# Performance work log

Hardware: AMD Instinct MI355X
Metric: run time of the kernel (lower is better)

The kernel has to match this reference:

```python
import jax, jax.numpy as jnp
import numpy as np

P = 16         # patch size
D = 192        # embed dim (vit_tiny)
NH = 3         # heads
DEPTH = 12
HID = 768      # mlp hidden = 4*D
NCLS = 1000
PCT = 0.25
EPS = 1e-6


def _ln(x, s, b):
    m = x.mean(-1, keepdims=True)
    v = ((x - m) ** 2).mean(-1, keepdims=True)
    return (x - m) * jax.lax.rsqrt(v + EPS) * s + b


def setup_inputs() -> dict:
    key = jax.random.key(0)
    ks = jax.random.split(key, 24)
    B, IMG = 64, 384
    std = 0.02
    d = {
        "magno_image": jax.random.normal(ks[0], (B, 3, IMG, IMG), jnp.float32),
        "line_drawing": jax.random.uniform(ks[1], (B, 1, IMG, IMG), jnp.float32),
        "conv_w": jax.random.normal(ks[2], (D, 3, P, P), jnp.float32) * std,
        "conv_b": jnp.zeros((D,), jnp.float32),
        "pos_embed": jax.random.normal(ks[3], (1, (IMG // P) ** 2 + 1, D), jnp.float32) * std,
        "cls_token": jax.random.normal(ks[4], (1, 1, D), jnp.float32) * std,
        "ln1_s": jnp.ones((DEPTH, D), jnp.float32),
        "ln1_b": jnp.zeros((DEPTH, D), jnp.float32),
        "qkv_w": jax.random.normal(ks[5], (DEPTH, D, 3 * D), jnp.float32) * std,
        "qkv_b": jnp.zeros((DEPTH, 3 * D), jnp.float32),
        "proj_w": jax.random.normal(ks[6], (DEPTH, D, D), jnp.float32) * std,
        "proj_b": jnp.zeros((DEPTH, D), jnp.float32),
        "ln2_s": jnp.ones((DEPTH, D), jnp.float32),
        "ln2_b": jnp.zeros((DEPTH, D), jnp.float32),
        "fc1_w": jax.random.normal(ks[7], (DEPTH, D, HID), jnp.float32) * std,
        "fc1_b": jnp.zeros((DEPTH, HID), jnp.float32),
        "fc2_w": jax.random.normal(ks[8], (DEPTH, HID, D), jnp.float32) * std,
        "fc2_b": jnp.zeros((DEPTH, D), jnp.float32),
        "normf_s": jnp.ones((D,), jnp.float32),
        "normf_b": jnp.zeros((D,), jnp.float32),
        "head_w": jax.random.normal(ks[9], (D, NCLS), jnp.float32) * std,
        "head_b": jnp.zeros((NCLS,), jnp.float32),
    }
    return d


def _forward(magno_image, line_drawing, conv_w, conv_b, pos_embed, cls_token,
             ln1_s, ln1_b, qkv_w, qkv_b, proj_w, proj_b, ln2_s, ln2_b,
             fc1_w, fc1_b, fc2_w, fc2_b, normf_s, normf_b, head_w, head_b):
    B, _, IMG, _ = magno_image.shape
    g = IMG // P
    N = g * g
    k = int(N * PCT)
    hd = D // NH

    # --- PatchImportanceScorer: avg-pool(patch_size) then flatten ---
    scores = line_drawing.reshape(B, g, P, g, P).mean(axis=(2, 4)).reshape(B, N)

    # --- patch embed (conv stride == kernel == reshaped matmul) ---
    x = magno_image.reshape(B, 3, g, P, g, P).transpose(0, 2, 4, 1, 3, 5)
    patches = x.reshape(B, N, 3 * P * P) @ conv_w.reshape(D, 3 * P * P).T + conv_b

    # --- top_k selection + gather of patches and pos-embed ---
    _, idx = jax.lax.top_k(scores, k)                      # (B, k)
    sel = jnp.take_along_axis(patches, idx[:, :, None], axis=1)
    pos = jnp.take_along_axis(
        jnp.broadcast_to(pos_embed[:, 1:, :], (B, N, D)), idx[:, :, None], axis=1)
    sel = sel + pos

    cls = jnp.broadcast_to(cls_token + pos_embed[:, :1, :], (B, 1, D))
    seq = jnp.concatenate([cls, sel], axis=1)              # (B, 1+k, D)
    S = 1 + k

    def block(h, p):
        l1s, l1b, qw, qb, pw, pb, l2s, l2b, f1w, f1b, f2w, f2b = p
        y = _ln(h, l1s, l1b)
        qkv = (y @ qw + qb).reshape(B, S, 3, NH, hd)
        q, kk, v = qkv[:, :, 0], qkv[:, :, 1], qkv[:, :, 2]  # (B,S,NH,hd)
        att = jnp.einsum('bqhd,bkhd->bhqk', q, kk) / np.sqrt(hd).astype(np.float32)
        att = jax.nn.softmax(att, axis=-1)
        o = jnp.einsum('bhqk,bkhd->bqhd', att, v).reshape(B, S, D)
        h = h + o @ pw + pb
        y = _ln(h, l2s, l2b)
        h = h + jax.nn.gelu(y @ f1w + f1b, approximate=False) @ f2w + f2b
        return h, None

    seq, _ = jax.lax.scan(block, seq, (ln1_s, ln1_b, qkv_w, qkv_b, proj_w, proj_b,
                                       ln2_s, ln2_b, fc1_w, fc1_b, fc2_w, fc2_b))
    seq = _ln(seq, normf_s, normf_b)
    return seq[:, 0] @ head_w + head_b


def reference(magno_image, line_drawing, conv_w, conv_b, pos_embed, cls_token,
              ln1_s, ln1_b, qkv_w, qkv_b, proj_w, proj_b, ln2_s, ln2_b,
              fc1_w, fc1_b, fc2_w, fc2_b, normf_s, normf_b, head_w, head_b):
    return _forward(magno_image, line_drawing, conv_w, conv_b, pos_embed, cls_token,
                    ln1_s, ln1_b, qkv_w, qkv_b, proj_w, proj_b, ln2_s, ln2_b,
                    fc1_w, fc1_b, fc2_w, fc2_b, normf_s, normf_b, head_w, head_b)
```

## Files before the change

kernel.cpp:

```cpp
#include <hip/hip_runtime.h>
#include <hip/hip_bf16.h>
#include <cmath>


#define Bsz   64
#define NPATCH 576
#define KSEL  144
#define SEQ   145
#define DIM   192
#define HIDN  768

typedef __bf16 bf16x8 __attribute__((ext_vector_type(8)));
typedef float  f32x4  __attribute__((ext_vector_type(4)));

__global__ __launch_bounds__(256) void scores_kernel(const float* __restrict__ line,
                                                     float* __restrict__ scores)
{
    int gp = blockIdx.x;
    int b = gp / NPATCH, p = gp % NPATCH;
    int gy = p / 24, gx = p % 24;
    int t = threadIdx.x, py = t >> 4, px = t & 15;
    float v = line[((size_t)b * 384 + gy * 16 + py) * 384 + gx * 16 + px];
    for (int off = 32; off; off >>= 1) v += __shfl_xor(v, off);
    __shared__ float red[4];
    if ((t & 63) == 0) red[t >> 6] = v;
    __syncthreads();
    if (t == 0) scores[gp] = (red[0] + red[1] + red[2] + red[3]) * (1.f / 256.f);
}

__global__ __launch_bounds__(256) void topk_kernel(const float* __restrict__ scores,
                                                   int* __restrict__ idx)
{
    int b = blockIdx.x;
    __shared__ float s[NPATCH];
    __shared__ unsigned char sel[NPATCH];
    for (int i = threadIdx.x; i < NPATCH; i += 256) s[i] = scores[b * NPATCH + i];
    __syncthreads();
    for (int i = threadIdx.x; i < NPATCH; i += 256) {
        float si = s[i];
        int cnt = 0;
        for (int j = 0; j < NPATCH; ++j) {
            float sj = s[j];
            cnt += (sj > si) || (sj == si && j < i);
        }
        sel[i] = (cnt < KSEL) ? 1 : 0;
    }
    __syncthreads();
    if (threadIdx.x == 0) {
        int slot = 0;
        for (int i = 0; i < NPATCH; ++i)
            if (sel[i]) idx[b * KSEL + slot++] = i;
    }
}

__global__ __launch_bounds__(256) void gather_kernel(const float* __restrict__ magno,
                                                     const int* __restrict__ idx,
                                                     __hip_bfloat16* __restrict__ selp)
{
    int bs = blockIdx.x;
    int b = bs / KSEL;
    int pi = idx[bs];
    int gy = pi / 24, gx = pi % 24;
    int t = threadIdx.x, py = t >> 4, px = t & 15;
    size_t src = ((size_t)b * 3 * 384 + gy * 16 + py) * 384 + gx * 16 + px;
    __hip_bfloat16* dst = &selp[(size_t)bs * 768];
#pragma unroll
    for (int c = 0; c < 3; ++c)
        dst[c * 256 + t] = __float2bfloat16(magno[src + (size_t)c * 384 * 384]);
}

__global__ __launch_bounds__(256) void convert_bf16_kernel(const float* __restrict__ src,
                                                           __hip_bfloat16* __restrict__ dst,
                                                           int n)
{
    int i = blockIdx.x * 256 + threadIdx.x;
    if (i < n) dst[i] = __float2bfloat16(src[i]);
}

__global__ __launch_bounds__(256) void transpose_w_kernel(const float* __restrict__ src,
                                                          __hip_bfloat16* __restrict__ dst,
                                                          int R, int C)
{
    __shared__ float t[32][33];
    size_t lo = (size_t)blockIdx.z * R * C;
    int r0 = blockIdx.y * 32, c0 = blockIdx.x * 32;
    int tx = threadIdx.x & 31, ty = threadIdx.x >> 5;
#pragma unroll
    for (int i = 0; i < 32; i += 8)
        t[ty + i][tx] = src[lo + (size_t)(r0 + ty + i) * C + c0 + tx];
    __syncthreads();
#pragma unroll
    for (int i = 0; i < 32; i += 8)
        dst[lo + (size_t)(c0 + ty + i) * R + r0 + tx] = __float2bfloat16(t[tx][ty + i]);
}

__global__ void cls_kernel(const float* __restrict__ cls, const float* __restrict__ pos,
                           float* __restrict__ h)
{
    int b = blockIdx.x, t = threadIdx.x;
    h[(size_t)b * SEQ * DIM + t] = cls[t] + pos[t];
}

__global__ __launch_bounds__(256) void ln_kernel(const float* __restrict__ x,
                                                 const float* __restrict__ s,
                                                 const float* __restrict__ bia,
                                                 __hip_bfloat16* __restrict__ y, int ntok)
{
    int w = threadIdx.x >> 6, lane = threadIdx.x & 63;
    int tok = blockIdx.x * 4 + w;
    if (tok >= ntok) return;
    const float* xp = &x[(size_t)tok * DIM];
    float x0 = xp[lane], x1 = xp[lane + 64], x2 = xp[lane + 128];
    float sum = x0 + x1 + x2;
    for (int off = 32; off; off >>= 1) sum += __shfl_xor(sum, off);
    float mean = sum * (1.f / 192.f);
    float d0 = x0 - mean, d1 = x1 - mean, d2 = x2 - mean;
    float vs = d0 * d0 + d1 * d1 + d2 * d2;
    for (int off = 32; off; off >>= 1) vs += __shfl_xor(vs, off);
    float rs = rsqrtf(vs * (1.f / 192.f) + 1e-6f);
    __hip_bfloat16* yp = &y[(size_t)tok * DIM];
    yp[lane]       = __float2bfloat16(d0 * rs * s[lane]       + bia[lane]);
    yp[lane + 64]  = __float2bfloat16(d1 * rs * s[lane + 64]  + bia[lane + 64]);
    yp[lane + 128] = __float2bfloat16(d2 * rs * s[lane + 128] + bia[lane + 128]);
}

template <int MODE>
__global__ __launch_bounds__(256) void gemm_bf16(const __hip_bfloat16* __restrict__ A,
                                                 const __hip_bfloat16* __restrict__ Wt,
                                                 const float* __restrict__ bias,
                                                 void* __restrict__ Cout,
                                                 int M, int N, int K,
                                                 const int* __restrict__ selidx,
                                                 const float* __restrict__ pos)
{
    __shared__ __align__(16) char As[8192];
    __shared__ __align__(16) char Bs[8192];
    const int tid = threadIdx.x;
    const int lane = tid & 63, wid = tid >> 6;
    const int wr = wid >> 1, wc = wid & 1;
    const int lr = lane & 15, lk = lane >> 4;
    const int m0 = blockIdx.y * 64, n0 = blockIdx.x * 64;
    f32x4 acc[2][2] = {};

    for (int k0 = 0; k0 < K; k0 += 64) {
#pragma unroll
        for (int it = 0; it < 2; ++it) {
            int chunk = it * 256 + tid;
            int r = chunk >> 3, g = chunk & 7;
            int loff = r * 128 + ((g ^ (r & 7)) * 16);
            *reinterpret_cast<uint4*>(As + loff) =
                *reinterpret_cast<const uint4*>(&A[(size_t)(m0 + r) * K + k0 + g * 8]);
            *reinterpret_cast<uint4*>(Bs + loff) =
                *reinterpret_cast<const uint4*>(&Wt[(size_t)(n0 + r) * K + k0 + g * 8]);
        }
        __syncthreads();
#pragma unroll
        for (int kc = 0; kc < 2; ++kc) {
            int g = kc * 4 + lk;
            bf16x8 af[2], bfr[2];
#pragma unroll
            for (int mi = 0; mi < 2; ++mi) {
                int r = wr * 32 + mi * 16 + lr;
                af[mi] = *reinterpret_cast<const bf16x8*>(As + r * 128 + ((g ^ (r & 7)) * 16));
            }
#pragma unroll
            for (int ni = 0; ni < 2; ++ni) {
                int r = wc * 32 + ni * 16 + lr;
                bfr[ni] = *reinterpret_cast<const bf16x8*>(Bs + r * 128 + ((g ^ (r & 7)) * 16));
            }
#pragma unroll
            for (int mi = 0; mi < 2; ++mi)
#pragma unroll
                for (int ni = 0; ni < 2; ++ni)
                    acc[mi][ni] = __builtin_amdgcn_mfma_f32_16x16x32_bf16(
                        af[mi], bfr[ni], acc[mi][ni], 0, 0, 0);
        }
        __syncthreads();
    }

#pragma unroll
    for (int mi = 0; mi < 2; ++mi)
#pragma unroll
    for (int ni = 0; ni < 2; ++ni)
#pragma unroll
    for (int j = 0; j < 4; ++j) {
        int row = m0 + wr * 32 + mi * 16 + (lane >> 4) * 4 + j;
        int col = n0 + wc * 32 + ni * 16 + (lane & 15);
        float v = acc[mi][ni][j] + bias[col];
        if (MODE == 0) {
            ((__hip_bfloat16*)Cout)[(size_t)row * N + col] = __float2bfloat16(v);
        } else if (MODE == 1) {
            ((float*)Cout)[(size_t)row * N + col] += v;
        } else if (MODE == 2) {
            ((__hip_bfloat16*)Cout)[(size_t)row * N + col] =
                __float2bfloat16(0.5f * v * (1.f + erff(v * 0.70710678118654752f)));
        } else {
            int bb2 = row / KSEL, ss = row % KSEL;
            int pi = selidx[row];
            v += pos[(size_t)(1 + pi) * DIM + col];
            ((float*)Cout)[((size_t)bb2 * SEQ + 1 + ss) * DIM + col] = v;
        }
    }
}

__global__ __launch_bounds__(256) void vtrans_kernel(const __hip_bfloat16* __restrict__ qkv,
                                                     __hip_bfloat16* __restrict__ Vt)
{
    const int b = blockIdx.x, h = blockIdx.y;
    __shared__ unsigned short lds[160][72];
    const int tid = threadIdx.x;
    for (int c = tid; c < 160 * 8; c += 256) {
        int s = c >> 3, g = c & 7;
        uint4 v = make_uint4(0, 0, 0, 0);
        if (s < SEQ)
            v = *reinterpret_cast<const uint4*>(
                &qkv[((size_t)b * SEQ + s) * 576 + 384 + h * 64 + g * 8]);
        *reinterpret_cast<uint4*>(&lds[s][g * 8]) = v;
    }
    __syncthreads();
    unsigned short* dst = (unsigned short*)&Vt[(size_t)(b * 3 + h) * 64 * 160];
    for (int e = tid; e < 64 * 160; e += 256) {
        int d = e / 160, s = e - d * 160;
        dst[e] = lds[s][d];
    }
}

__global__ __launch_bounds__(128) void attn3_kernel(const __hip_bfloat16* __restrict__ qkv,
                                                    const __hip_bfloat16* __restrict__ Vt,
                                                    __hip_bfloat16* __restrict__ o)
{
    const int b = blockIdx.y;
    const int h = blockIdx.x / 5, qt = blockIdx.x % 5;
    const int tid = threadIdx.x;
    const int wq = tid >> 6, lane = tid & 63;
    const int lr = lane & 15, lg = lane >> 4;
    __shared__ __hip_bfloat16 Ps[2][16][168];

    const size_t qbase = (size_t)b * SEQ * 576;
    const int q0 = qt * 32 + wq * 16;

    bf16x8 aq[2];
#pragma unroll
    for (int ks = 0; ks < 2; ++ks)
        aq[ks] = *reinterpret_cast<const bf16x8*>(
            &qkv[qbase + (size_t)(q0 + lr) * 576 + h * 64 + ks * 32 + lg * 8]);

    f32x4 sc[10];
#pragma unroll
    for (int nf = 0; nf < 10; ++nf) sc[nf] = (f32x4){0.f, 0.f, 0.f, 0.f};
#pragma unroll
    for (int nf = 0; nf < 10; ++nf) {
        int key = nf * 16 + lr;
#pragma unroll
        for (int ks = 0; ks < 2; ++ks) {
            bf16x8 bk = *reinterpret_cast<const bf16x8*>(
                &qkv[qbase + (size_t)key * 576 + 192 + h * 64 + ks * 32 + lg * 8]);
            sc[nf] = __builtin_amdgcn_mfma_f32_16x16x32_bf16(aq[ks], bk, sc[nf], 0, 0, 0);
        }
    }

    float mx[4] = {-1e30f, -1e30f, -1e30f, -1e30f};
#pragma unroll
    for (int nf = 0; nf < 10; ++nf) {
        bool valid = nf * 16 + lr < SEQ;
#pragma unroll
        for (int j = 0; j < 4; ++j) {
            float v = valid ? sc[nf][j] * 0.125f : -1e30f;
            sc[nf][j] = v;
            mx[j] = fmaxf(mx[j], v);
        }
    }
#pragma unroll
    for (int j = 0; j < 4; ++j)
        for (int off = 1; off < 16; off <<= 1)
            mx[j] = fmaxf(mx[j], __shfl_xor(mx[j], off));
    float sm[4] = {0.f, 0.f, 0.f, 0.f};
#pragma unroll
    for (int nf = 0; nf < 10; ++nf)
#pragma unroll
        for (int j = 0; j < 4; ++j) {
            float p = __expf(sc[nf][j] - mx[j]);
            sc[nf][j] = p;
            sm[j] += p;
        }
#pragma unroll
    for (int j = 0; j < 4; ++j) {
        for (int off = 1; off < 16; off <<= 1) sm[j] += __shfl_xor(sm[j], off);
        sm[j] = 1.f / sm[j];
    }
#pragma unroll
    for (int nf = 0; nf < 10; ++nf) {
        int key = nf * 16 + lr;
#pragma unroll
        for (int j = 0; j < 4; ++j)
            Ps[wq][lg * 4 + j][key] = __float2bfloat16(sc[nf][j] * sm[j]);
    }
    __syncthreads();

    const __hip_bfloat16* vtb = &Vt[(size_t)(b * 3 + h) * 64 * 160];
    f32x4 oacc[4];
#pragma unroll
    for (int nf = 0; nf < 4; ++nf) oacc[nf] = (f32x4){0.f, 0.f, 0.f, 0.f};
#pragma unroll
    for (int ks = 0; ks < 5; ++ks) {
        bf16x8 ap = *reinterpret_cast<const bf16x8*>(&Ps[wq][lr][ks * 32 + lg * 8]);
#pragma unroll
        for (int nf = 0; nf < 4; ++nf) {
            bf16x8 bv = *reinterpret_cast<const bf16x8*>(
                &vtb[(size_t)(nf * 16 + lr) * 160 + ks * 32 + lg * 8]);
            oacc[nf] = __builtin_amdgcn_mfma_f32_16x16x32_bf16(ap, bv, oacc[nf], 0, 0, 0);
        }
    }
#pragma unroll
    for (int nf = 0; nf < 4; ++nf)
#pragma unroll
        for (int j = 0; j < 4; ++j) {
            int q = q0 + lg * 4 + j;
            if (q < SEQ)
                o[((size_t)b * SEQ + q) * DIM + h * 64 + nf * 16 + lr] =
                    __float2bfloat16(oacc[nf][j]);
        }
}

__global__ __launch_bounds__(256) void head_kernel(const float* __restrict__ h,
                                                   const float* __restrict__ nfs,
                                                   const float* __restrict__ nfb,
                                                   const float* __restrict__ hw,
                                                   const float* __restrict__ hb,
                                                   float* __restrict__ out)
{
    int b = blockIdx.x, t = threadIdx.x;
    __shared__ float y[DIM];
    __shared__ float red[4];
    float x = (t < DIM) ? h[(size_t)b * SEQ * DIM + t] : 0.f;
    float sum = x;
    for (int off = 32; off; off >>= 1) sum += __shfl_xor(sum, off);
    if ((t & 63) == 0) red[t >> 6] = sum;
    __syncthreads();
    float mean = (red[0] + red[1] + red[2] + red[3]) * (1.f / 192.f);
    __syncthreads();
    float d = (t < DIM) ? (x - mean) : 0.f;
    float v = d * d;
    for (int off = 32; off; off >>= 1) v += __shfl_xor(v, off);
    if ((t & 63) == 0) red[t >> 6] = v;
    __syncthreads();
    float var = (red[0] + red[1] + red[2] + red[3]) * (1.f / 192.f);
    float rs = rsqrtf(var + 1e-6f);
    if (t < DIM) y[t] = d * rs * nfs[t] + nfb[t];
    __syncthreads();
    for (int n = t; n < 1000; n += 256) {
        float acc = hb[n];
#pragma unroll 8
        for (int k = 0; k < DIM; ++k)
            acc = fmaf(y[k], hw[(size_t)k * 1000 + n], acc);
        out[(size_t)b * 1000 + n] = acc;
    }
}

extern "C" void kernel_launch(void* const* d_in, const int* in_sizes, int n_in,
                              void* d_out, int out_size, void* d_ws, size_t ws_size,
                              hipStream_t stream)
{
    const float* magno  = (const float*)d_in[0];
    const float* line   = (const float*)d_in[1];
    const float* conv_w = (const float*)d_in[2];
    const float* conv_b = (const float*)d_in[3];
    const float* pos    = (const float*)d_in[4];
    const float* cls    = (const float*)d_in[5];
    const float* ln1_s  = (const float*)d_in[6];
    const float* ln1_b  = (const float*)d_in[7];
    const float* qkv_w  = (const float*)d_in[8];
    const float* qkv_b  = (const float*)d_in[9];
    const float* proj_w = (const float*)d_in[10];
    const float* proj_b = (const float*)d_in[11];
    const float* ln2_s  = (const float*)d_in[12];
    const float* ln2_b  = (const float*)d_in[13];
    const float* fc1_w  = (const float*)d_in[14];
    const float* fc1_b  = (const float*)d_in[15];
    const float* fc2_w  = (const float*)d_in[16];
    const float* fc2_b  = (const float*)d_in[17];
    const float* normf_s = (const float*)d_in[18];
    const float* normf_b = (const float*)d_in[19];
    const float* head_w = (const float*)d_in[20];
    const float* head_b = (const float*)d_in[21];
    float* out = (float*)d_out;
    (void)in_sizes; (void)n_in; (void)out_size; (void)ws_size;

    char* ws = (char*)d_ws;
    int*            idx     = (int*)            (ws + 0);
    float*          h       = (float*)          (ws + 147456);
    __hip_bfloat16* y       = (__hip_bfloat16*) (ws + 7274496);
    __hip_bfloat16* qkv     = (__hip_bfloat16*) (ws + 10838016);
    __hip_bfloat16* Vt      = (__hip_bfloat16*) (ws + 21528576);
    __hip_bfloat16* tbuf    = (__hip_bfloat16*) (ws + 25460736);
    __hip_bfloat16* wt_qkv  = (__hip_bfloat16*) (ws + 39714816);
    __hip_bfloat16* wt_proj = (__hip_bfloat16*) (ws + 42369024);
    __hip_bfloat16* wt_fc1  = (__hip_bfloat16*) (ws + 43253760);
    __hip_bfloat16* wt_fc2  = (__hip_bfloat16*) (ws + 46792704);
    float*          scoresbuf = (float*)qkv;
    __hip_bfloat16* convT     = y;
    __hip_bfloat16* selp      = tbuf;

    transpose_w_kernel<<<dim3(18, 6, 12), 256, 0, stream>>>(qkv_w, wt_qkv, DIM, 576);
    transpose_w_kernel<<<dim3(6, 6, 12),  256, 0, stream>>>(proj_w, wt_proj, DIM, DIM);
    transpose_w_kernel<<<dim3(24, 6, 12), 256, 0, stream>>>(fc1_w, wt_fc1, DIM, HIDN);
    transpose_w_kernel<<<dim3(6, 24, 12), 256, 0, stream>>>(fc2_w, wt_fc2, HIDN, DIM);
    convert_bf16_kernel<<<576, 256, 0, stream>>>(conv_w, convT, DIM * 768);

    scores_kernel<<<Bsz * NPATCH, 256, 0, stream>>>(line, scoresbuf);
    topk_kernel<<<Bsz, 256, 0, stream>>>(scoresbuf, idx);
    gather_kernel<<<Bsz * KSEL, 256, 0, stream>>>(magno, idx, selp);
    cls_kernel<<<Bsz, DIM, 0, stream>>>(cls, pos, h);
    gemm_bf16<3><<<dim3(3, 144), 256, 0, stream>>>(selp, convT, conv_b, h,
                                                   9216, DIM, 768, idx, pos);

    const int ntok = Bsz * SEQ;
    for (int l = 0; l < 12; ++l) {
        ln_kernel<<<ntok / 4, 256, 0, stream>>>(h, ln1_s + l * DIM, ln1_b + l * DIM, y, ntok);
        gemm_bf16<0><<<dim3(9, 145), 256, 0, stream>>>(y, wt_qkv + (size_t)l * 576 * DIM,
                                                       qkv_b + l * 576, qkv,
                                                       ntok, 576, DIM, nullptr, nullptr);
        vtrans_kernel<<<dim3(Bsz, 3), 256, 0, stream>>>(qkv, Vt);
        attn3_kernel<<<dim3(15, Bsz), 128, 0, stream>>>(qkv, Vt, y);
        gemm_bf16<1><<<dim3(3, 145), 256, 0, stream>>>(y, wt_proj + (size_t)l * DIM * DIM,
                                                       proj_b + l * DIM, h,
                                                       ntok, DIM, DIM, nullptr, nullptr);
        ln_kernel<<<ntok / 4, 256, 0, stream>>>(h, ln2_s + l * DIM, ln2_b + l * DIM, y, ntok);
        gemm_bf16<2><<<dim3(12, 145), 256, 0, stream>>>(y, wt_fc1 + (size_t)l * HIDN * DIM,
                                                        fc1_b + l * HIDN, tbuf,
                                                        ntok, HIDN, DIM, nullptr, nullptr);
        gemm_bf16<1><<<dim3(3, 145), 256, 0, stream>>>(tbuf, wt_fc2 + (size_t)l * DIM * HIDN,
                                                       fc2_b + l * DIM, h,
                                                       ntok, DIM, HIDN, nullptr, nullptr);
    }
    head_kernel<<<Bsz, 256, 0, stream>>>(h, normf_s, normf_b, head_w, head_b, out);
}
```

Measured before the change: 1.005 ms.

## Fuse residual GEMMs with LayerNorm and write V transposed from the QKV GEMM

Replaces the proj and fc2 residual GEMMs with a full-row (N=192) GEMM kernel that adds the residual and bias and then computes the next LayerNorm in its epilogue. This removes the standalone ln_kernel launches and their extra pass over h. The V slice of the QKV projection now comes from a separate GEMM that writes directly into the transposed Vt layout, which drops the vtrans kernel and the V part of the qkv buffer. Top-k writes each index into its rank slot in parallel instead of compacting serially in one thread; this changes the index order to score rank rather than patch position. The trade-off is 145 large-tile blocks for the fused GEMMs, which gives low occupancy, plus scattered 2-byte stores into Vt.

```diff
diff --git a/kernel.cpp b/kernel.cpp
--- a/kernel.cpp
+++ b/kernel.cpp
@@ -33,7 +33,6 @@
 {
     int b = blockIdx.x;
     __shared__ float s[NPATCH];
-    __shared__ unsigned char sel[NPATCH];
     for (int i = threadIdx.x; i < NPATCH; i += 256) s[i] = scores[b * NPATCH + i];
     __syncthreads();
     for (int i = threadIdx.x; i < NPATCH; i += 256) {
@@ -43,13 +42,7 @@
             float sj = s[j];
             cnt += (sj > si) || (sj == si && j < i);
         }
-        sel[i] = (cnt < KSEL) ? 1 : 0;
-    }
-    __syncthreads();
-    if (threadIdx.x == 0) {
-        int slot = 0;
-        for (int i = 0; i < NPATCH; ++i)
-            if (sel[i]) idx[b * KSEL + slot++] = i;
+        if (cnt < KSEL) idx[b * KSEL + cnt] = i;
     }
 }
 
@@ -189,8 +182,6 @@
         float v = acc[mi][ni][j] + bias[col];
         if (MODE == 0) {
             ((__hip_bfloat16*)Cout)[(size_t)row * N + col] = __float2bfloat16(v);
-        } else if (MODE == 1) {
-            ((float*)Cout)[(size_t)row * N + col] += v;
         } else if (MODE == 2) {
             ((__hip_bfloat16*)Cout)[(size_t)row * N + col] =
                 __float2bfloat16(0.5f * v * (1.f + erff(v * 0.70710678118654752f)));
@@ -203,29 +194,172 @@
     }
 }
 
-__global__ __launch_bounds__(256) void vtrans_kernel(const __hip_bfloat16* __restrict__ qkv,
-                                                     __hip_bfloat16* __restrict__ Vt)
-{
-    const int b = blockIdx.x, h = blockIdx.y;
-    __shared__ unsigned short lds[160][72];
+__global__ __launch_bounds__(256) void gemm_vt(const __hip_bfloat16* __restrict__ A,
+                                               const __hip_bfloat16* __restrict__ Wt,
+                                               const float* __restrict__ bias,
+                                               __hip_bfloat16* __restrict__ Vt)
+{
+    __shared__ __align__(16) char As[8192];
+    __shared__ __align__(16) char Bs[8192];
     const int tid = threadIdx.x;
-    for (int c = tid; c < 160 * 8; c += 256) {
-        int s = c >> 3, g = c & 7;
-        uint4 v = make_uint4(0, 0, 0, 0);
-        if (s < SEQ)
-            v = *reinterpret_cast<const uint4*>(
-                &qkv[((size_t)b * SEQ + s) * 576 + 384 + h * 64 + g * 8]);
-        *reinterpret_cast<uint4*>(&lds[s][g * 8]) = v;
-    }
-    __syncthreads();
-    unsigned short* dst = (unsigned short*)&Vt[(size_t)(b * 3 + h) * 64 * 160];
-    for (int e = tid; e < 64 * 160; e += 256) {
-        int d = e / 160, s = e - d * 160;
-        dst[e] = lds[s][d];
-    }
-}
-
-__global__ __launch_bounds__(128) void attn3_kernel(const __hip_bfloat16* __restrict__ qkv,
+    const int lane = tid & 63, wid = tid >> 6;
+    const int wr = wid >> 1, wc = wid & 1;
+    const int lr = lane & 15, lk = lane >> 4;
+    const int m0 = blockIdx.y * 64, n0 = blockIdx.x * 64;
+    const int K = DIM;
+    f32x4 acc[2][2] = {};
+
+    for (int k0 = 0; k0 < K; k0 += 64) {
+#pragma unroll
+        for (int it = 0; it < 2; ++it) {
+            int chunk = it * 256 + tid;
+            int r = chunk >> 3, g = chunk & 7;
+            int loff = r * 128 + ((g ^ (r & 7)) * 16);
+            *reinterpret_cast<uint4*>(As + loff) =
+                *reinterpret_cast<const uint4*>(&A[(size_t)(m0 + r) * K + k0 + g * 8]);
+            *reinterpret_cast<uint4*>(Bs + loff) =
+                *reinterpret_cast<const uint4*>(&Wt[(size_t)(n0 + r) * K + k0 + g * 8]);
+        }
+        __syncthreads();
+#pragma unroll
+        for (int kc = 0; kc < 2; ++kc) {
+            int g = kc * 4 + lk;
+            bf16x8 af[2], bfr[2];
+#pragma unroll
+            for (int mi = 0; mi < 2; ++mi) {
+                int r = wr * 32 + mi * 16 + lr;
+                af[mi] = *reinterpret_cast<const bf16x8*>(As + r * 128 + ((g ^ (r & 7)) * 16));
+            }
+#pragma unroll
+            for (int ni = 0; ni < 2; ++ni) {
+                int r = wc * 32 + ni * 16 + lr;
+                bfr[ni] = *reinterpret_cast<const bf16x8*>(Bs + r * 128 + ((g ^ (r & 7)) * 16));
+            }
+#pragma unroll
+            for (int mi = 0; mi < 2; ++mi)
+#pragma unroll
+                for (int ni = 0; ni < 2; ++ni)
+                    acc[mi][ni] = __builtin_amdgcn_mfma_f32_16x16x32_bf16(
+                        af[mi], bfr[ni], acc[mi][ni], 0, 0, 0);
+        }
+        __syncthreads();
+    }
+
+#pragma unroll
+    for (int mi = 0; mi < 2; ++mi)
+#pragma unroll
+    for (int ni = 0; ni < 2; ++ni)
+#pragma unroll
+    for (int j = 0; j < 4; ++j) {
+        int row = m0 + wr * 32 + mi * 16 + (lane >> 4) * 4 + j;
+        int c   = n0 + wc * 32 + ni * 16 + (lane & 15);
+        float v = acc[mi][ni][j] + bias[c];
+        int b = row / SEQ, s = row - b * SEQ;
+        Vt[((size_t)(b * 3 + (c >> 6)) * 64 + (c & 63)) * 160 + s] = __float2bfloat16(v);
+    }
+}
+
+template <bool DO_LN>
+__global__ __launch_bounds__(256) void gemm_res_ln(const __hip_bfloat16* __restrict__ A,
+                                                   const __hip_bfloat16* __restrict__ Wt,
+                                                   const float* __restrict__ bias,
+                                                   float* __restrict__ h,
+                                                   const float* __restrict__ ls,
+                                                   const float* __restrict__ lb,
+                                                   __hip_bfloat16* __restrict__ y,
+                                                   int K)
+{
+    __shared__ __align__(16) char As[8192];
+    __shared__ __align__(16) char Bs[24576];
+    const int tid = threadIdx.x;
+    const int lane = tid & 63, w = tid >> 6;
+    const int lr = lane & 15, lg = lane >> 4;
+    const int m0 = blockIdx.x * 64;
+    f32x4 acc[12] = {};
+
+    for (int k0 = 0; k0 < K; k0 += 64) {
+        {
+            int chunk = tid;
+#pragma unroll
+            for (int it = 0; it < 2; ++it, chunk += 256) {
+                int r = chunk >> 3, g = chunk & 7;
+                *reinterpret_cast<uint4*>(As + r * 128 + ((g ^ (r & 7)) * 16)) =
+                    *reinterpret_cast<const uint4*>(&A[(size_t)(m0 + r) * K + k0 + g * 8]);
+            }
+        }
+        {
+            int chunk = tid;
+#pragma unroll
+            for (int it = 0; it < 6; ++it, chunk += 256) {
+                int r = chunk >> 3, g = chunk & 7;
+                *reinterpret_cast<uint4*>(Bs + r * 128 + ((g ^ (r & 7)) * 16)) =
+                    *reinterpret_cast<const uint4*>(&Wt[(size_t)r * K + k0 + g * 8]);
+            }
+        }
+        __syncthreads();
+#pragma unroll
+        for (int kc = 0; kc < 2; ++kc) {
+            int g = kc * 4 + lg;
+            int ar = w * 16 + lr;
+            bf16x8 af = *reinterpret_cast<const bf16x8*>(As + ar * 128 + ((g ^ (ar & 7)) * 16));
+#pragma unroll
+            for (int nf = 0; nf < 12; ++nf) {
+                int br = nf * 16 + lr;
+                bf16x8 bfv = *reinterpret_cast<const bf16x8*>(Bs + br * 128 + ((g ^ (br & 7)) * 16));
+                acc[nf] = __builtin_amdgcn_mfma_f32_16x16x32_bf16(af, bfv, acc[nf], 0, 0, 0);
+            }
+        }
+        __syncthreads();
+    }
+
+    float v[12][4];
+    float sum[4] = {0.f, 0.f, 0.f, 0.f};
+#pragma unroll
+    for (int nf = 0; nf < 12; ++nf) {
+        int col = nf * 16 + lr;
+#pragma unroll
+        for (int j = 0; j < 4; ++j) {
+            int row = m0 + w * 16 + lg * 4 + j;
+            float t = acc[nf][j] + bias[col] + h[(size_t)row * DIM + col];
+            v[nf][j] = t;
+            h[(size_t)row * DIM + col] = t;
+            sum[j] += t;
+        }
+    }
+    if (DO_LN) {
+#pragma unroll
+        for (int j = 0; j < 4; ++j)
+            for (int off = 1; off < 16; off <<= 1) sum[j] += __shfl_xor(sum[j], off);
+        float mean[4], sq[4] = {0.f, 0.f, 0.f, 0.f};
+#pragma unroll
+        for (int j = 0; j < 4; ++j) mean[j] = sum[j] * (1.f / 192.f);
+#pragma unroll
+        for (int nf = 0; nf < 12; ++nf)
+#pragma unroll
+            for (int j = 0; j < 4; ++j) {
+                float d = v[nf][j] - mean[j];
+                sq[j] += d * d;
+            }
+#pragma unroll
+        for (int j = 0; j < 4; ++j) {
+            for (int off = 1; off < 16; off <<= 1) sq[j] += __shfl_xor(sq[j], off);
+            sq[j] = rsqrtf(sq[j] * (1.f / 192.f) + 1e-6f);
+        }
+#pragma unroll
+        for (int nf = 0; nf < 12; ++nf) {
+            int col = nf * 16 + lr;
+            float sc = ls[col], bc = lb[col];
+#pragma unroll
+            for (int j = 0; j < 4; ++j) {
+                int row = m0 + w * 16 + lg * 4 + j;
+                y[(size_t)row * DIM + col] =
+                    __float2bfloat16((v[nf][j] - mean[j]) * sq[j] * sc + bc);
+            }
+        }
+    }
+}
+
+__global__ __launch_bounds__(128) void attn3_kernel(const __hip_bfloat16* __restrict__ qk,
                                                     const __hip_bfloat16* __restrict__ Vt,
                                                     __hip_bfloat16* __restrict__ o)
 {
@@ -236,14 +370,14 @@
     const int lr = lane & 15, lg = lane >> 4;
     __shared__ __hip_bfloat16 Ps[2][16][168];
 
-    const size_t qbase = (size_t)b * SEQ * 576;
+    const size_t qbase = (size_t)b * SEQ * 384;
     const int q0 = qt * 32 + wq * 16;
 
     bf16x8 aq[2];
 #pragma unroll
     for (int ks = 0; ks < 2; ++ks)
         aq[ks] = *reinterpret_cast<const bf16x8*>(
-            &qkv[qbase + (size_t)(q0 + lr) * 576 + h * 64 + ks * 32 + lg * 8]);
+            &qk[qbase + (size_t)(q0 + lr) * 384 + h * 64 + ks * 32 + lg * 8]);
 
     f32x4 sc[10];
 #pragma unroll
@@ -254,7 +388,7 @@
 #pragma unroll
         for (int ks = 0; ks < 2; ++ks) {
             bf16x8 bk = *reinterpret_cast<const bf16x8*>(
-                &qkv[qbase + (size_t)key * 576 + 192 + h * 64 + ks * 32 + lg * 8]);
+                &qk[qbase + (size_t)key * 384 + 192 + h * 64 + ks * 32 + lg * 8]);
             sc[nf] = __builtin_amdgcn_mfma_f32_16x16x32_bf16(aq[ks], bk, sc[nf], 0, 0, 0);
         }
     }
@@ -390,17 +524,18 @@
     int*            idx     = (int*)            (ws + 0);
     float*          h       = (float*)          (ws + 147456);
     __hip_bfloat16* y       = (__hip_bfloat16*) (ws + 7274496);
-    __hip_bfloat16* qkv     = (__hip_bfloat16*) (ws + 10838016);
-    __hip_bfloat16* Vt      = (__hip_bfloat16*) (ws + 21528576);
-    __hip_bfloat16* tbuf    = (__hip_bfloat16*) (ws + 25460736);
-    __hip_bfloat16* wt_qkv  = (__hip_bfloat16*) (ws + 39714816);
-    __hip_bfloat16* wt_proj = (__hip_bfloat16*) (ws + 42369024);
-    __hip_bfloat16* wt_fc1  = (__hip_bfloat16*) (ws + 43253760);
-    __hip_bfloat16* wt_fc2  = (__hip_bfloat16*) (ws + 46792704);
-    float*          scoresbuf = (float*)qkv;
+    __hip_bfloat16* qk      = (__hip_bfloat16*) (ws + 10838016);
+    __hip_bfloat16* Vt      = (__hip_bfloat16*) (ws + 17965056);
+    __hip_bfloat16* tbuf    = (__hip_bfloat16*) (ws + 21897216);
+    __hip_bfloat16* wt_qkv  = (__hip_bfloat16*) (ws + 36151296);
+    __hip_bfloat16* wt_proj = (__hip_bfloat16*) (ws + 38805504);
+    __hip_bfloat16* wt_fc1  = (__hip_bfloat16*) (ws + 39690240);
+    __hip_bfloat16* wt_fc2  = (__hip_bfloat16*) (ws + 43229184);
+    float*          scoresbuf = (float*)qk;
     __hip_bfloat16* convT     = y;
     __hip_bfloat16* selp      = tbuf;
 
+    hipMemsetAsync(Vt, 0, 3932160, stream);
     transpose_w_kernel<<<dim3(18, 6, 12), 256, 0, stream>>>(qkv_w, wt_qkv, DIM, 576);
     transpose_w_kernel<<<dim3(6, 6, 12),  256, 0, stream>>>(proj_w, wt_proj, DIM, DIM);
     transpose_w_kernel<<<dim3(24, 6, 12), 256, 0, stream>>>(fc1_w, wt_fc1, DIM, HIDN);
@@ -415,23 +550,29 @@
                                                    9216, DIM, 768, idx, pos);
 
     const int ntok = Bsz * SEQ;
+    ln_kernel<<<ntok / 4, 256, 0, stream>>>(h, ln1_s, ln1_b, y, ntok);
     for (int l = 0; l < 12; ++l) {
-        ln_kernel<<<ntok / 4, 256, 0, stream>>>(h, ln1_s + l * DIM, ln1_b + l * DIM, y, ntok);
-        gemm_bf16<0><<<dim3(9, 145), 256, 0, stream>>>(y, wt_qkv + (size_t)l * 576 * DIM,
-                                                       qkv_b + l * 576, qkv,
-                                                       ntok, 576, DIM, nullptr, nullptr);
-        vtrans_kernel<<<dim3(Bsz, 3), 256, 0, stream>>>(qkv, Vt);
-        attn3_kernel<<<dim3(15, Bsz), 128, 0, stream>>>(qkv, Vt, y);
-        gemm_bf16<1><<<dim3(3, 145), 256, 0, stream>>>(y, wt_proj + (size_t)l * DIM * DIM,
-                                                       proj_b + l * DIM, h,
-                                                       ntok, DIM, DIM, nullptr, nullptr);
-        ln_kernel<<<ntok / 4, 256, 0, stream>>>(h, ln2_s + l * DIM, ln2_b + l * DIM, y, ntok);
+        gemm_bf16<0><<<dim3(6, 145), 256, 0, stream>>>(y, wt_qkv + (size_t)l * 576 * DIM,
+                                                       qkv_b + l * 576, qk,
+                                                       ntok, 384, DIM, nullptr, nullptr);
+        gemm_vt<<<dim3(3, 145), 256, 0, stream>>>(y, wt_qkv + (size_t)l * 576 * DIM + 384 * DIM,
+                                                  qkv_b + l * 576 + 384, Vt);
+        attn3_kernel<<<dim3(15, Bsz), 128, 0, stream>>>(qk, Vt, y);
+        gemm_res_ln<true><<<145, 256, 0, stream>>>(y, wt_proj + (size_t)l * DIM * DIM,
+                                                   proj_b + l * DIM, h,
+                                                   ln2_s + l * DIM, ln2_b + l * DIM, y, DIM);
         gemm_bf16<2><<<dim3(12, 145), 256, 0, stream>>>(y, wt_fc1 + (size_t)l * HIDN * DIM,
                                                         fc1_b + l * HIDN, tbuf,
                                                         ntok, HIDN, DIM, nullptr, nullptr);
-        gemm_bf16<1><<<dim3(3, 145), 256, 0, stream>>>(tbuf, wt_fc2 + (size_t)l * DIM * HIDN,
+        if (l < 11)
+            gemm_res_ln<true><<<145, 256, 0, stream>>>(tbuf, wt_fc2 + (size_t)l * DIM * HIDN,
                                                        fc2_b + l * DIM, h,
-                                                       ntok, DIM, HIDN, nullptr, nullptr);
+                                                       ln1_s + (l + 1) * DIM, ln1_b + (l + 1) * DIM,
+                                                       y, HIDN);
+        else
+            gemm_res_ln<false><<<145, 256, 0, stream>>>(tbuf, wt_fc2 + (size_t)l * DIM * HIDN,
+                                                        fc2_b + l * DIM, h,
+                                                        nullptr, nullptr, y, HIDN);
     }
     head_kernel<<<Bsz, 256, 0, stream>>>(h, normf_s, normf_b, head_w, head_b, out);
 }
```

Result: faster. 969.9 us (-3.5%).
